# Performance work log

Hardware: AMD Instinct MI355X
Metric: run time of the kernel (lower is better)

## Reference

```python
import jax, jax.numpy as jnp
import numpy as np

TOP_K = 2


def setup_inputs() -> dict:
    key = jax.random.key(0)
    ks = jax.random.split(key, 5)
    T, H, I, E = 4096, 2048, 4096, 8
    scale = 0.02
    return {
        "hidden_states": jax.random.normal(ks[0], (T, H), dtype=jnp.float32),
        "router_logits": jax.random.normal(ks[1], (T, E), dtype=jnp.float32),
        "w1": jax.random.normal(ks[2], (E, I, H), dtype=jnp.float32) * scale,
        "w3": jax.random.normal(ks[3], (E, I, H), dtype=jnp.float32) * scale,
        "w2": jax.random.normal(ks[4], (E, H, I), dtype=jnp.float32) * scale,
    }


def reference(hidden_states, router_logits, w1, w3, w2):
    # hidden_states: [T, H], router_logits: [T, E]
    E = w1.shape[0]
    # Top-k routing with softmax renormalization over the selected logits.
    topk_vals, topk_idx = jax.lax.top_k(router_logits, TOP_K)  # [T, K]
    routing_weights = jax.nn.softmax(topk_vals, axis=-1)       # [T, K]
    # combine[t, e] = sum of routing weights of slots that picked expert e
    combine = jnp.sum(
        jnp.where(topk_idx[:, :, None] == jnp.arange(E)[None, None, :],
                  routing_weights[:, :, None], 0.0),
        axis=1)  # [T, E]
    out = jnp.zeros_like(hidden_states)
    for e in range(E):  # fixed small structural loop over experts
        gate = hidden_states @ w1[e].T        # [T, I]
        up = hidden_states @ w3[e].T          # [T, I]
        y = (jax.nn.silu(gate) * up) @ w2[e].T  # [T, H]
        out = out + combine[:, e, None] * y
    return out
```

## Files before the change

### kernel.cpp

```cpp
#include <hip/hip_runtime.h>
#include <stdint.h>

#define T_TOK 4096
#define H_DIM 2048
#define I_DIM 4096
#define N_EXP 8

typedef __attribute__((ext_vector_type(8))) short bf16x8;
typedef __attribute__((ext_vector_type(4))) float f32x4;
typedef __attribute__((ext_vector_type(8))) unsigned short u16x8;

__device__ __forceinline__ unsigned short f2bf(float x) {
    union { float f; unsigned u; } v; v.f = x;
    unsigned r = v.u + 0x7FFF + ((v.u >> 16) & 1);
    return (unsigned short)(r >> 16);
}

__device__ __forceinline__ u16x8 cvt8(float4 a, float4 b) {
    u16x8 o;
    o[0] = f2bf(a.x); o[1] = f2bf(a.y); o[2] = f2bf(a.z); o[3] = f2bf(a.w);
    o[4] = f2bf(b.x); o[5] = f2bf(b.y); o[6] = f2bf(b.z); o[7] = f2bf(b.w);
    return o;
}

__device__ __forceinline__ void async_cp16(const void* g, const unsigned short* lds_base) {
    __builtin_amdgcn_global_load_lds(
        (const __attribute__((address_space(1))) unsigned*)g,
        (__attribute__((address_space(3))) unsigned*)(unsigned)(uintptr_t)lds_base,
        16, 0, 0);
}

__global__ void routing_kernel(const float* __restrict__ logits,
                               int* __restrict__ counts, int* __restrict__ offsets,
                               int* __restrict__ btok, float* __restrict__ bw,
                               int* __restrict__ tok2slot) {
    __shared__ int s_cnt[N_EXP];
    __shared__ int s_off[N_EXP];
    __shared__ int s_cur[N_EXP];
    const int tid = threadIdx.x;
    if (tid < N_EXP) s_cnt[tid] = 0;
    __syncthreads();

    int e0a[16], e1a[16]; float w0a[16], w1a[16];
    #pragma unroll
    for (int it = 0; it < 16; ++it) {
        int t = tid + it * 256;
        float l[8];
        #pragma unroll
        for (int e = 0; e < 8; ++e) l[e] = logits[t * 8 + e];
        int b0 = 0; float v0 = l[0];
        #pragma unroll
        for (int e = 1; e < 8; ++e) if (l[e] > v0) { v0 = l[e]; b0 = e; }
        int b1 = (b0 == 0) ? 1 : 0; float v1 = l[b1];
        #pragma unroll
        for (int e = 0; e < 8; ++e) if (e != b0 && l[e] > v1) { v1 = l[e]; b1 = e; }
        float w0 = 1.0f / (1.0f + __expf(v1 - v0));
        e0a[it] = b0; e1a[it] = b1; w0a[it] = w0; w1a[it] = 1.0f - w0;
        atomicAdd(&s_cnt[b0], 1);
        atomicAdd(&s_cnt[b1], 1);
    }
    __syncthreads();
    if (tid == 0) {
        int acc = 0;
        for (int e = 0; e < N_EXP; ++e) { s_off[e] = acc; s_cur[e] = acc; acc += s_cnt[e]; }
    }
    __syncthreads();
    if (tid < N_EXP) { counts[tid] = s_cnt[tid]; offsets[tid] = s_off[tid]; }
    #pragma unroll
    for (int it = 0; it < 16; ++it) {
        int t = tid + it * 256;
        int p0 = atomicAdd(&s_cur[e0a[it]], 1);
        btok[p0] = t; bw[p0] = w0a[it];
        int p1 = atomicAdd(&s_cur[e1a[it]], 1);
        btok[p1] = t; bw[p1] = w1a[it];
        tok2slot[2 * t] = p0;
        tok2slot[2 * t + 1] = p1;
    }
}

__global__ void cvt_kernel(const float* __restrict__ x, unsigned short* __restrict__ xb) {
    int i = blockIdx.x * blockDim.x + threadIdx.x;
    float4 a = ((const float4*)x)[2 * i];
    float4 b = ((const float4*)x)[2 * i + 1];
    ((u16x8*)xb)[i] = cvt8(a, b);
}


__global__ __launch_bounds__(512, 2)
void gemm1p_kernel(const unsigned short* __restrict__ Xb,
                   const float* __restrict__ W1,
                   const float* __restrict__ W3,
                   const int* __restrict__ counts,
                   const int* __restrict__ offsets,
                   const int* __restrict__ btok,
                   unsigned short* __restrict__ hbuf) {
    const int e = blockIdx.z;
    const int ne = counts[e];
    const int mt = blockIdx.y;
    if (mt * 256 >= ne) return;
    const int nt = blockIdx.x;
    const int off = offsets[e];

    __shared__ unsigned short sA[4][256 * 32];
    __shared__ unsigned short sB1[4][128 * 32];
    __shared__ unsigned short sB3[4][128 * 32];

    const int tid = threadIdx.x;
    const int lane = tid & 63;
    const int wv = tid >> 6;
    const int wm = (wv >> 1) << 6;
    const int wn = (wv & 1) << 6;
    const int q = lane >> 4;
    const int c = lane & 15;
    const int xq = q ^ ((c >> 1) & 3);

    const int aoff = (wm + c) * 32 + xq * 8;
    const int boff = (wn + c) * 32 + xq * 8;

    const int srow = wv * 16 + (lane >> 2);
    const int sg = (lane & 3) ^ ((lane >> 3) & 3);

    int sl0 = mt * 256 + srow;        if (sl0 >= ne) sl0 = ne - 1;
    int sl1 = mt * 256 + srow + 128;  if (sl1 >= ne) sl1 = ne - 1;
    const int tok0 = btok[off + sl0];
    const int tok1 = btok[off + sl1];

    const unsigned short* gA0 = Xb + (size_t)tok0 * H_DIM + sg * 8;
    const unsigned short* gA1 = Xb + (size_t)tok1 * H_DIM + sg * 8;
    const size_t wrow = (size_t)e * I_DIM + nt * 128 + srow;
    const float* gW1 = W1 + wrow * H_DIM + (lane & 3) * 8;
    const float* gW3 = W3 + wrow * H_DIM + (lane & 3) * 8;
    const int bwro = srow * 32 + sg * 8;

    const int dofsA0 = wv * 512;
    const int dofsA1 = 4096 + wv * 512;

    f32x4 accg[4][4], accu[4][4];
    const f32x4 zero = {0.0f, 0.0f, 0.0f, 0.0f};
    #pragma unroll
    for (int i = 0; i < 4; ++i)
        #pragma unroll
        for (int j = 0; j < 4; ++j) { accg[i][j] = zero; accu[i][j] = zero; }

    {
        float4 a0 = *(const float4*)(gW1);
        float4 a1 = *(const float4*)(gW1 + 4);
        float4 b0 = *(const float4*)(gW3);
        float4 b1 = *(const float4*)(gW3 + 4);
        float4 c0 = *(const float4*)(gW1 + 32);
        float4 c1 = *(const float4*)(gW1 + 36);
        float4 d0 = *(const float4*)(gW3 + 32);
        float4 d1 = *(const float4*)(gW3 + 36);
        *(u16x8*)(&sB1[0][bwro]) = cvt8(a0, a1);
        *(u16x8*)(&sB3[0][bwro]) = cvt8(b0, b1);
        *(u16x8*)(&sB1[1][bwro]) = cvt8(c0, c1);
        *(u16x8*)(&sB3[1][bwro]) = cvt8(d0, d1);
    }
    async_cp16(gA0,      &sA[0][dofsA0]);
    async_cp16(gA1,      &sA[0][dofsA1]);
    async_cp16(gA0 + 32, &sA[1][dofsA0]);
    async_cp16(gA1 + 32, &sA[1][dofsA1]);

    const int NT = H_DIM / 32;
    float4 rc0, rc1, rc2, rc3, rn0, rn1, rn2, rn3;
    rc0 = *(const float4*)(gW1 + 64);
    rc1 = *(const float4*)(gW1 + 68);
    rc2 = *(const float4*)(gW3 + 64);
    rc3 = *(const float4*)(gW3 + 68);

    asm volatile("s_waitcnt lgkmcnt(0)" ::: "memory");
    asm volatile("s_waitcnt vmcnt(6)" ::: "memory");
    __builtin_amdgcn_s_barrier();
    __builtin_amdgcn_sched_barrier(0);

#define G1_PHASE(H, RC0, RC1, RC2, RC3, RN0, RN1, RN2, RN3)                                          \
    {                                                                                                \
        const int cs = (H) & 3;                                                                      \
        if ((H) + 3 < NT) {                                                                          \
            const float* p1 = gW1 + (size_t)((H) + 3) * 32;                                          \
            const float* p3 = gW3 + (size_t)((H) + 3) * 32;                                          \
            RN0 = *(const float4*)(p1);                                                              \
            RN1 = *(const float4*)(p1 + 4);                                                          \
            RN2 = *(const float4*)(p3);                                                              \
            RN3 = *(const float4*)(p3 + 4);                                                          \
        }                                                                                            \
        bf16x8 af[4], b1f[4], b3f[4];                                                                \
        _Pragma("unroll")                                                                            \
        for (int i = 0; i < 4; ++i) af[i]  = *(const bf16x8*)(&sA[cs][aoff + i * 512]);              \
        _Pragma("unroll")                                                                            \
        for (int j = 0; j < 4; ++j) b1f[j] = *(const bf16x8*)(&sB1[cs][boff + j * 512]);             \
        _Pragma("unroll")                                                                            \
        for (int j = 0; j < 4; ++j) b3f[j] = *(const bf16x8*)(&sB3[cs][boff + j * 512]);             \
        if ((H) + 2 < NT) {                                                                          \
            const int ns = ((H) + 2) & 3;                                                            \
            async_cp16(gA0 + ((H) + 2) * 32, &sA[ns][dofsA0]);                                       \
            async_cp16(gA1 + ((H) + 2) * 32, &sA[ns][dofsA1]);                                       \
        }                                                                                            \
        __builtin_amdgcn_sched_barrier(0);                                                           \
        __builtin_amdgcn_s_setprio(1);                                                               \
        _Pragma("unroll")                                                                            \
        for (int i = 0; i < 4; ++i)                                                                  \
            _Pragma("unroll")                                                                        \
            for (int j = 0; j < 4; ++j)                                                              \
                accg[i][j] = __builtin_amdgcn_mfma_f32_16x16x32_bf16(af[i], b1f[j], accg[i][j], 0, 0, 0); \
        _Pragma("unroll")                                                                            \
        for (int i = 0; i < 4; ++i)                                                                  \
            _Pragma("unroll")                                                                        \
            for (int j = 0; j < 4; ++j)                                                              \
                accu[i][j] = __builtin_amdgcn_mfma_f32_16x16x32_bf16(af[i], b3f[j], accu[i][j], 0, 0, 0); \
        __builtin_amdgcn_s_setprio(0);                                                               \
        if ((H) + 2 < NT) {                                                                          \
            const int ns = ((H) + 2) & 3;                                                            \
            *(u16x8*)(&sB1[ns][bwro]) = cvt8(RC0, RC1);                                              \
            *(u16x8*)(&sB3[ns][bwro]) = cvt8(RC2, RC3);                                              \
        }                                                                                            \
        if ((H) + 1 < NT) {                                                                          \
            asm volatile("s_waitcnt lgkmcnt(0)" ::: "memory");                                       \
            if ((H) + 3 < NT)      asm volatile("s_waitcnt vmcnt(6)" ::: "memory");                  \
            else if ((H) + 2 < NT) asm volatile("s_waitcnt vmcnt(2)" ::: "memory");                  \
            else                   asm volatile("s_waitcnt vmcnt(0)" ::: "memory");                  \
            __builtin_amdgcn_s_barrier();                                                            \
            __builtin_amdgcn_sched_barrier(0);                                                       \
        }                                                                                            \
    }

    for (int h = 0; h < NT; h += 2) {
        G1_PHASE(h,     rc0, rc1, rc2, rc3, rn0, rn1, rn2, rn3);
        G1_PHASE(h + 1, rn0, rn1, rn2, rn3, rc0, rc1, rc2, rc3);
    }
#undef G1_PHASE

    #pragma unroll
    for (int i = 0; i < 4; ++i) {
        #pragma unroll
        for (int r = 0; r < 4; ++r) {
            int mloc = wm + i * 16 + q * 4 + r;
            int slot = mt * 256 + mloc;
            if (slot < ne) {
                size_t rowbase = (size_t)(off + slot) * I_DIM + nt * 128 + wn;
                #pragma unroll
                for (int j = 0; j < 4; ++j) {
                    float g = accg[i][j][r];
                    float u = accu[i][j][r];
                    float val = (g / (1.0f + __expf(-g))) * u;
                    hbuf[rowbase + j * 16 + c] = f2bf(val);
                }
            }
        }
    }
}

__global__ __launch_bounds__(512, 2)
void gemm2p_kernel(const unsigned short* __restrict__ hbuf,
                   const float* __restrict__ W2,
                   const int* __restrict__ counts,
                   const int* __restrict__ offsets,
                   float* __restrict__ ybuf) {
    const int e = blockIdx.z;
    const int ne = counts[e];
    const int mt = blockIdx.y;
    if (mt * 256 >= ne) return;
    const int nt = blockIdx.x;
    const int off = offsets[e];

    __shared__ unsigned short sA[4][256 * 32];
    __shared__ unsigned short sB[4][256 * 32];

    const int tid = threadIdx.x;
    const int lane = tid & 63;
    const int wv = tid >> 6;
    const int wm = (wv >> 2) << 7;
    const int wn = (wv & 3) << 6;
    const int q = lane >> 4;
    const int c = lane & 15;
    const int xq = q ^ ((c >> 1) & 3);

    const int aoff = (wm + c) * 32 + xq * 8;
    const int boff = (wn + c) * 32 + xq * 8;

    const int srow = wv * 16 + (lane >> 2);
    const int sg = (lane & 3) ^ ((lane >> 3) & 3);

    int slot0 = mt * 256 + srow;        if (slot0 >= ne) slot0 = ne - 1;
    int slot1 = mt * 256 + srow + 128;  if (slot1 >= ne) slot1 = ne - 1;
    const unsigned short* gA0 = hbuf + (size_t)(off + slot0) * I_DIM + sg * 8;
    const unsigned short* gA1 = hbuf + (size_t)(off + slot1) * I_DIM + sg * 8;
    const size_t wrow = (size_t)e * H_DIM + nt * 256 + srow;
    const float* gB0 = W2 + wrow * I_DIM + (lane & 3) * 8;
    const float* gB1 = gB0 + (size_t)128 * I_DIM;
    const int bwro = srow * 32 + sg * 8;

    const int dofsA0 = wv * 512;
    const int dofsA1 = 4096 + wv * 512;

    f32x4 acc[8][4];
    const f32x4 zero = {0.0f, 0.0f, 0.0f, 0.0f};
    #pragma unroll
    for (int i = 0; i < 8; ++i)
        #pragma unroll
        for (int j = 0; j < 4; ++j) acc[i][j] = zero;

    {
        float4 a0 = *(const float4*)(gB0);
        float4 a1 = *(const float4*)(gB0 + 4);
        float4 b0 = *(const float4*)(gB1);
        float4 b1 = *(const float4*)(gB1 + 4);
        float4 c0 = *(const float4*)(gB0 + 32);
        float4 c1 = *(const float4*)(gB0 + 36);
        float4 d0 = *(const float4*)(gB1 + 32);
        float4 d1 = *(const float4*)(gB1 + 36);
        *(u16x8*)(&sB[0][bwro])        = cvt8(a0, a1);
        *(u16x8*)(&sB[0][bwro + 4096]) = cvt8(b0, b1);
        *(u16x8*)(&sB[1][bwro])        = cvt8(c0, c1);
        *(u16x8*)(&sB[1][bwro + 4096]) = cvt8(d0, d1);
    }
    async_cp16(gA0,      &sA[0][dofsA0]);
    async_cp16(gA1,      &sA[0][dofsA1]);
    async_cp16(gA0 + 32, &sA[1][dofsA0]);
    async_cp16(gA1 + 32, &sA[1][dofsA1]);

    const int NT = I_DIM / 32;
    float4 rc0, rc1, rc2, rc3, rn0, rn1, rn2, rn3;
    rc0 = *(const float4*)(gB0 + 64);
    rc1 = *(const float4*)(gB0 + 68);
    rc2 = *(const float4*)(gB1 + 64);
    rc3 = *(const float4*)(gB1 + 68);

    asm volatile("s_waitcnt lgkmcnt(0)" ::: "memory");
    asm volatile("s_waitcnt vmcnt(6)" ::: "memory");
    __builtin_amdgcn_s_barrier();
    __builtin_amdgcn_sched_barrier(0);

#define G2_PHASE(H, RC0, RC1, RC2, RC3, RN0, RN1, RN2, RN3)                                          \
    {                                                                                                \
        const int cs = (H) & 3;                                                                      \
        if ((H) + 3 < NT) {                                                                          \
            const float* p0 = gB0 + (size_t)((H) + 3) * 32;                                          \
            const float* p1 = gB1 + (size_t)((H) + 3) * 32;                                          \
            RN0 = *(const float4*)(p0);                                                              \
            RN1 = *(const float4*)(p0 + 4);                                                          \
            RN2 = *(const float4*)(p1);                                                              \
            RN3 = *(const float4*)(p1 + 4);                                                          \
        }                                                                                            \
        bf16x8 af[8], bfr[4];                                                                        \
        _Pragma("unroll")                                                                            \
        for (int i = 0; i < 8; ++i) af[i]  = *(const bf16x8*)(&sA[cs][aoff + i * 512]);              \
        _Pragma("unroll")                                                                            \
        for (int j = 0; j < 4; ++j) bfr[j] = *(const bf16x8*)(&sB[cs][boff + j * 512]);              \
        if ((H) + 2 < NT) {                                                                          \
            const int ns = ((H) + 2) & 3;                                                            \
            async_cp16(gA0 + ((H) + 2) * 32, &sA[ns][dofsA0]);                                       \
            async_cp16(gA1 + ((H) + 2) * 32, &sA[ns][dofsA1]);                                       \
        }                                                                                            \
        __builtin_amdgcn_sched_barrier(0);                                                           \
        __builtin_amdgcn_s_setprio(1);                                                               \
        _Pragma("unroll")                                                                            \
        for (int i = 0; i < 8; ++i)                                                                  \
            _Pragma("unroll")                                                                        \
            for (int j = 0; j < 4; ++j)                                                              \
                acc[i][j] = __builtin_amdgcn_mfma_f32_16x16x32_bf16(af[i], bfr[j], acc[i][j], 0, 0, 0); \
        __builtin_amdgcn_s_setprio(0);                                                               \
        if ((H) + 2 < NT) {                                                                          \
            const int ns = ((H) + 2) & 3;                                                            \
            *(u16x8*)(&sB[ns][bwro])        = cvt8(RC0, RC1);                                        \
            *(u16x8*)(&sB[ns][bwro + 4096]) = cvt8(RC2, RC3);                                        \
        }                                                                                            \
        if ((H) + 1 < NT) {                                                                          \
            asm volatile("s_waitcnt lgkmcnt(0)" ::: "memory");                                       \
            if ((H) + 3 < NT)      asm volatile("s_waitcnt vmcnt(6)" ::: "memory");                  \
            else if ((H) + 2 < NT) asm volatile("s_waitcnt vmcnt(2)" ::: "memory");                  \
            else                   asm volatile("s_waitcnt vmcnt(0)" ::: "memory");                  \
            __builtin_amdgcn_s_barrier();                                                            \
            __builtin_amdgcn_sched_barrier(0);                                                       \
        }                                                                                            \
    }

    for (int h = 0; h < NT; h += 2) {
        G2_PHASE(h,     rc0, rc1, rc2, rc3, rn0, rn1, rn2, rn3);
        G2_PHASE(h + 1, rn0, rn1, rn2, rn3, rc0, rc1, rc2, rc3);
    }
#undef G2_PHASE

    #pragma unroll
    for (int i = 0; i < 8; ++i) {
        #pragma unroll
        for (int r = 0; r < 4; ++r) {
            int mloc = wm + i * 16 + q * 4 + r;
            int slot = mt * 256 + mloc;
            if (slot < ne) {
                float* obase = ybuf + (size_t)(off + slot) * H_DIM + nt * 256 + wn;
                #pragma unroll
                for (int j = 0; j < 4; ++j)
                    obase[j * 16 + c] = acc[i][j][r];
            }
        }
    }
}

__global__ void combine_kernel(const float* __restrict__ ybuf,
                               const float* __restrict__ bw,
                               const int* __restrict__ tok2slot,
                               float* __restrict__ out) {
    int i = blockIdx.x * blockDim.x + threadIdx.x;
    int t = i >> 9;
    int h4 = i & 511;
    int p0 = tok2slot[2 * t], p1 = tok2slot[2 * t + 1];
    float w0 = bw[p0], w1 = bw[p1];
    float4 a = ((const float4*)(ybuf + (size_t)p0 * H_DIM))[h4];
    float4 b = ((const float4*)(ybuf + (size_t)p1 * H_DIM))[h4];
    float4 o;
    o.x = w0 * a.x + w1 * b.x;
    o.y = w0 * a.y + w1 * b.y;
    o.z = w0 * a.z + w1 * b.z;
    o.w = w0 * a.w + w1 * b.w;
    ((float4*)(out + (size_t)t * H_DIM))[h4] = o;
}


__global__ __launch_bounds__(256, 2)
void gemm1_kernel(const unsigned short* __restrict__ Xb,
                  const float* __restrict__ W1,
                  const float* __restrict__ W3,
                  const int* __restrict__ counts,
                  const int* __restrict__ offsets,
                  const int* __restrict__ btok,
                  unsigned short* __restrict__ hbuf) {
    const int e = blockIdx.z;
    const int ne = counts[e];
    const int mt = blockIdx.y;
    if (mt * 128 >= ne) return;
    const int nt = blockIdx.x;
    const int off = offsets[e];

    __shared__ unsigned short sA[128][32];
    __shared__ unsigned short sB1[128][32];
    __shared__ unsigned short sB3[128][32];
    __shared__ int s_tok[128];

    const int tid = threadIdx.x;
    if (tid < 128) {
        int slot = mt * 128 + tid;
        s_tok[tid] = (slot < ne) ? btok[off + slot] : -1;
    }

    const float* __restrict__ pB1 = W1 + (size_t)e * I_DIM * H_DIM + (size_t)(nt * 128) * H_DIM;
    const float* __restrict__ pB3 = W3 + (size_t)e * I_DIM * H_DIM + (size_t)(nt * 128) * H_DIM;

    const int lane = tid & 63;
    const int wv = tid >> 6;
    const int wm = (wv >> 1) << 6;
    const int wn = (wv & 1) << 6;
    const int q = lane >> 4;
    const int c = lane & 15;

    f32x4 accg[4][4], accu[4][4];
    const f32x4 zero = {0.0f, 0.0f, 0.0f, 0.0f};
    #pragma unroll
    for (int i = 0; i < 4; ++i)
        #pragma unroll
        for (int j = 0; j < 4; ++j) { accg[i][j] = zero; accu[i][j] = zero; }

    const int srow = tid >> 2;
    const int schunk = (tid & 3) * 8;

    for (int kt = 0; kt < H_DIM; kt += 32) {
        __syncthreads();
        #pragma unroll
        for (int p = 0; p < 2; ++p) {
            int r = srow + p * 64;
            int tok = s_tok[r];
            u16x8 av = {0, 0, 0, 0, 0, 0, 0, 0};
            if (tok >= 0)
                av = *(const u16x8*)(Xb + (size_t)tok * H_DIM + kt + schunk);
            *(u16x8*)(&sA[r][schunk]) = av;

            const float* b1 = pB1 + (size_t)r * H_DIM + kt + schunk;
            *(u16x8*)(&sB1[r][schunk]) = cvt8(*(const float4*)(b1), *(const float4*)(b1 + 4));

            const float* b3 = pB3 + (size_t)r * H_DIM + kt + schunk;
            *(u16x8*)(&sB3[r][schunk]) = cvt8(*(const float4*)(b3), *(const float4*)(b3 + 4));
        }
        __syncthreads();

        bf16x8 af[4], b1f[4], b3f[4];
        #pragma unroll
        for (int i = 0; i < 4; ++i)
            af[i] = *(const bf16x8*)(&sA[wm + i * 16 + c][q * 8]);
        #pragma unroll
        for (int j = 0; j < 4; ++j) {
            b1f[j] = *(const bf16x8*)(&sB1[wn + j * 16 + c][q * 8]);
            b3f[j] = *(const bf16x8*)(&sB3[wn + j * 16 + c][q * 8]);
        }
        #pragma unroll
        for (int i = 0; i < 4; ++i)
            #pragma unroll
            for (int j = 0; j < 4; ++j) {
                accg[i][j] = __builtin_amdgcn_mfma_f32_16x16x32_bf16(af[i], b1f[j], accg[i][j], 0, 0, 0);
                accu[i][j] = __builtin_amdgcn_mfma_f32_16x16x32_bf16(af[i], b3f[j], accu[i][j], 0, 0, 0);
            }
    }

    #pragma unroll
    for (int i = 0; i < 4; ++i) {
        #pragma unroll
        for (int r = 0; r < 4; ++r) {
            int mloc = wm + i * 16 + q * 4 + r;
            int slot = mt * 128 + mloc;
            if (slot < ne) {
                size_t rowbase = (size_t)(off + slot) * I_DIM + nt * 128 + wn;
                #pragma unroll
                for (int j = 0; j < 4; ++j) {
                    float g = accg[i][j][r];
                    float u = accu[i][j][r];
                    float val = (g / (1.0f + __expf(-g))) * u;
                    hbuf[rowbase + j * 16 + c] = f2bf(val);
                }
            }
        }
    }
}

__global__ __launch_bounds__(256, 2)
void gemm2_kernel(const unsigned short* __restrict__ hbuf,
                  const float* __restrict__ W2,
                  const int* __restrict__ counts,
                  const int* __restrict__ offsets,
                  const int* __restrict__ btok,
                  const float* __restrict__ bw,
                  float* __restrict__ out) {
    const int e = blockIdx.z;
    const int ne = counts[e];
    const int mt = blockIdx.y;
    if (mt * 128 >= ne) return;
    const int nt = blockIdx.x;
    const int off = offsets[e];

    __shared__ unsigned short sA[128][32];
    __shared__ unsigned short sB[128][32];

    const int tid = threadIdx.x;
    const int lane = tid & 63;
    const int wv = tid >> 6;
    const int wm = (wv >> 1) << 6;
    const int wn = (wv & 1) << 6;
    const int q = lane >> 4;
    const int c = lane & 15;

    const float* __restrict__ pB = W2 + (size_t)e * H_DIM * I_DIM + (size_t)(nt * 128) * I_DIM;

    f32x4 acc[4][4];
    const f32x4 zero = {0.0f, 0.0f, 0.0f, 0.0f};
    #pragma unroll
    for (int i = 0; i < 4; ++i)
        #pragma unroll
        for (int j = 0; j < 4; ++j) acc[i][j] = zero;

    const int srow = tid >> 2;
    const int schunk = (tid & 3) * 8;

    for (int kt = 0; kt < I_DIM; kt += 32) {
        __syncthreads();
        #pragma unroll
        for (int p = 0; p < 2; ++p) {
            int r = srow + p * 64;
            int slot = mt * 128 + r;
            u16x8 av = {0, 0, 0, 0, 0, 0, 0, 0};
            if (slot < ne)
                av = *(const u16x8*)(hbuf + (size_t)(off + slot) * I_DIM + kt + schunk);
            *(u16x8*)(&sA[r][schunk]) = av;

            const float* b = pB + (size_t)r * I_DIM + kt + schunk;
            *(u16x8*)(&sB[r][schunk]) = cvt8(*(const float4*)(b), *(const float4*)(b + 4));
        }
        __syncthreads();

        bf16x8 af[4], bfr[4];
        #pragma unroll
        for (int i = 0; i < 4; ++i)
            af[i] = *(const bf16x8*)(&sA[wm + i * 16 + c][q * 8]);
        #pragma unroll
        for (int j = 0; j < 4; ++j)
            bfr[j] = *(const bf16x8*)(&sB[wn + j * 16 + c][q * 8]);
        #pragma unroll
        for (int i = 0; i < 4; ++i)
            #pragma unroll
            for (int j = 0; j < 4; ++j)
                acc[i][j] = __builtin_amdgcn_mfma_f32_16x16x32_bf16(af[i], bfr[j], acc[i][j], 0, 0, 0);
    }

    #pragma unroll
    for (int i = 0; i < 4; ++i) {
        #pragma unroll
        for (int r = 0; r < 4; ++r) {
            int mloc = wm + i * 16 + q * 4 + r;
            int slot = mt * 128 + mloc;
            if (slot < ne) {
                int tok = btok[off + slot];
                float wgt = bw[off + slot];
                float* obase = out + (size_t)tok * H_DIM + nt * 128 + wn;
                #pragma unroll
                for (int j = 0; j < 4; ++j)
                    atomicAdd(obase + j * 16 + c, wgt * acc[i][j][r]);
            }
        }
    }
}


extern "C" void kernel_launch(void* const* d_in, const int* in_sizes, int n_in,
                              void* d_out, int out_size, void* d_ws, size_t ws_size,
                              hipStream_t stream) {
    const float* hs = (const float*)d_in[0];
    const float* rl = (const float*)d_in[1];
    const float* w1 = (const float*)d_in[2];
    const float* w3 = (const float*)d_in[3];
    const float* w2 = (const float*)d_in[4];
    float* out = (float*)d_out;

    char* ws = (char*)d_ws;
    int*   counts   = (int*)(ws);
    int*   offsets  = (int*)(ws + 256);
    int*   btok     = (int*)(ws + 4096);
    float* bw       = (float*)(ws + 36864);
    int*   tok2slot = (int*)(ws + 69632);

    const size_t MB = 1ull << 20;
    const size_t NEED_A = 146 * MB;

    if (ws_size >= NEED_A) {
        unsigned short* Xb   = (unsigned short*)(ws + 1 * MB);
        unsigned short* hbuf = (unsigned short*)(ws + 17 * MB);
        float*          ybuf = (float*)(ws + 81 * MB);

        routing_kernel<<<1, 256, 0, stream>>>(rl, counts, offsets, btok, bw, tok2slot);

        cvt_kernel<<<(T_TOK * H_DIM / 8) / 256, 256, 0, stream>>>(hs, Xb);

        gemm1p_kernel<<<dim3(I_DIM / 128, 32, N_EXP), 512, 0, stream>>>(
            Xb, w1, w3, counts, offsets, btok, hbuf);

        gemm2p_kernel<<<dim3(H_DIM / 256, 32, N_EXP), 512, 0, stream>>>(
            hbuf, w2, counts, offsets, ybuf);

        combine_kernel<<<(T_TOK * (H_DIM / 4)) / 256, 256, 0, stream>>>(
            ybuf, bw, tok2slot, out);
    } else {
        unsigned short* Xb   = (unsigned short*)(ws + 1 * MB);
        unsigned short* hbuf = (unsigned short*)(ws + 32 * MB);

        hipMemsetAsync(out, 0, (size_t)T_TOK * H_DIM * sizeof(float), stream);

        routing_kernel<<<1, 256, 0, stream>>>(rl, counts, offsets, btok, bw, tok2slot);

        cvt_kernel<<<(T_TOK * H_DIM / 8) / 256, 256, 0, stream>>>(hs, Xb);

        gemm1_kernel<<<dim3(I_DIM / 128, T_TOK / 128, N_EXP), 256, 0, stream>>>(
            Xb, w1, w3, counts, offsets, btok, hbuf);

        gemm2_kernel<<<dim3(H_DIM / 128, T_TOK / 128, N_EXP), 256, 0, stream>>>(
            hbuf, w2, counts, offsets, btok, bw, out);
    }
}
```

Before: 1.308 ms.

## Shrink MoE GEMM tiles to 128x128 with 256 threads and triple-buffered LDS

Both grouped expert GEMMs move from 512-thread blocks with 256-row token tiles to 256-thread blocks with 128x128 output tiles. The LDS ring drops from four stages to three, and the pipeline is reordered so the fp32-to-bf16 weight conversion is written to LDS at the start of each phase instead of after the MFMAs. The aim is more blocks and better occupancy, plus less wasted work on partially filled expert tiles. In exchange, each fp32 weight tile is fetched and converted twice as often per token, which raises weight traffic from global memory.

```diff
diff --git a/kernel.cpp b/kernel.cpp
--- a/kernel.cpp
+++ b/kernel.cpp
@@ -86,7 +86,7 @@
 }
 
 
-__global__ __launch_bounds__(512, 2)
+__global__ __launch_bounds__(256, 2)
 void gemm1p_kernel(const unsigned short* __restrict__ Xb,
                    const float* __restrict__ W1,
                    const float* __restrict__ W3,
@@ -97,13 +97,13 @@
     const int e = blockIdx.z;
     const int ne = counts[e];
     const int mt = blockIdx.y;
-    if (mt * 256 >= ne) return;
+    if (mt * 128 >= ne) return;
     const int nt = blockIdx.x;
     const int off = offsets[e];
 
-    __shared__ unsigned short sA[4][256 * 32];
-    __shared__ unsigned short sB1[4][128 * 32];
-    __shared__ unsigned short sB3[4][128 * 32];
+    __shared__ unsigned short sA[3][128 * 32];
+    __shared__ unsigned short sB1[3][128 * 32];
+    __shared__ unsigned short sB3[3][128 * 32];
 
     const int tid = threadIdx.x;
     const int lane = tid & 63;
@@ -117,23 +117,25 @@
     const int aoff = (wm + c) * 32 + xq * 8;
     const int boff = (wn + c) * 32 + xq * 8;
 
-    const int srow = wv * 16 + (lane >> 2);
-    const int sg = (lane & 3) ^ ((lane >> 3) & 3);
-
-    int sl0 = mt * 256 + srow;        if (sl0 >= ne) sl0 = ne - 1;
-    int sl1 = mt * 256 + srow + 128;  if (sl1 >= ne) sl1 = ne - 1;
-    const int tok0 = btok[off + sl0];
-    const int tok1 = btok[off + sl1];
-
-    const unsigned short* gA0 = Xb + (size_t)tok0 * H_DIM + sg * 8;
-    const unsigned short* gA1 = Xb + (size_t)tok1 * H_DIM + sg * 8;
-    const size_t wrow = (size_t)e * I_DIM + nt * 128 + srow;
-    const float* gW1 = W1 + wrow * H_DIM + (lane & 3) * 8;
-    const float* gW3 = W3 + wrow * H_DIM + (lane & 3) * 8;
-    const int bwro = srow * 32 + sg * 8;
-
+    const int arow = wv * 16 + (lane >> 2);
+    const int sgA = (lane & 3) ^ ((lane >> 3) & 3);
+
+    int sl0 = mt * 128 + arow;       if (sl0 >= ne) sl0 = ne - 1;
+    int sl1 = mt * 128 + arow + 64;  if (sl1 >= ne) sl1 = ne - 1;
+    const unsigned short* gA0 = Xb + (size_t)btok[off + sl0] * H_DIM + sgA * 8;
+    const unsigned short* gA1 = Xb + (size_t)btok[off + sl1] * H_DIM + sgA * 8;
     const int dofsA0 = wv * 512;
-    const int dofsA1 = 4096 + wv * 512;
+    const int dofsA1 = 2048 + wv * 512;
+
+    const int brow = tid >> 2;
+    const int sgB = (tid & 3) ^ ((tid >> 3) & 3);
+    const size_t wrow = (size_t)e * I_DIM + nt * 128 + brow;
+    const float* gW1  = W1 + wrow * H_DIM + (tid & 3) * 8;
+    const float* gW1b = gW1 + (size_t)64 * H_DIM;
+    const float* gW3  = W3 + wrow * H_DIM + (tid & 3) * 8;
+    const float* gW3b = gW3 + (size_t)64 * H_DIM;
+    const int bwro  = brow * 32 + sgB * 8;
+    const int bwro2 = bwro + 2048;
 
     f32x4 accg[4][4], accu[4][4];
     const f32x4 zero = {0.0f, 0.0f, 0.0f, 0.0f};
@@ -142,59 +144,63 @@
         #pragma unroll
         for (int j = 0; j < 4; ++j) { accg[i][j] = zero; accu[i][j] = zero; }
 
-    {
-        float4 a0 = *(const float4*)(gW1);
-        float4 a1 = *(const float4*)(gW1 + 4);
-        float4 b0 = *(const float4*)(gW3);
-        float4 b1 = *(const float4*)(gW3 + 4);
-        float4 c0 = *(const float4*)(gW1 + 32);
-        float4 c1 = *(const float4*)(gW1 + 36);
-        float4 d0 = *(const float4*)(gW3 + 32);
-        float4 d1 = *(const float4*)(gW3 + 36);
-        *(u16x8*)(&sB1[0][bwro]) = cvt8(a0, a1);
-        *(u16x8*)(&sB3[0][bwro]) = cvt8(b0, b1);
-        *(u16x8*)(&sB1[1][bwro]) = cvt8(c0, c1);
-        *(u16x8*)(&sB3[1][bwro]) = cvt8(d0, d1);
+    float4 w0, w1, w2, w3, w4, w5, w6, w7;
+
+    #pragma unroll
+    for (int h = 0; h < 2; ++h) {
+        const float* p1  = gW1  + h * 32;
+        const float* p1b = gW1b + h * 32;
+        const float* p3  = gW3  + h * 32;
+        const float* p3b = gW3b + h * 32;
+        *(u16x8*)(&sB1[h][bwro])  = cvt8(((const float4*)p1)[0],  ((const float4*)p1)[1]);
+        *(u16x8*)(&sB1[h][bwro2]) = cvt8(((const float4*)p1b)[0], ((const float4*)p1b)[1]);
+        *(u16x8*)(&sB3[h][bwro])  = cvt8(((const float4*)p3)[0],  ((const float4*)p3)[1]);
+        *(u16x8*)(&sB3[h][bwro2]) = cvt8(((const float4*)p3b)[0], ((const float4*)p3b)[1]);
     }
     async_cp16(gA0,      &sA[0][dofsA0]);
     async_cp16(gA1,      &sA[0][dofsA1]);
     async_cp16(gA0 + 32, &sA[1][dofsA0]);
     async_cp16(gA1 + 32, &sA[1][dofsA1]);
-
-    const int NT = H_DIM / 32;
-    float4 rc0, rc1, rc2, rc3, rn0, rn1, rn2, rn3;
-    rc0 = *(const float4*)(gW1 + 64);
-    rc1 = *(const float4*)(gW1 + 68);
-    rc2 = *(const float4*)(gW3 + 64);
-    rc3 = *(const float4*)(gW3 + 68);
+    w0 = ((const float4*)(gW1  + 64))[0]; w1 = ((const float4*)(gW1  + 64))[1];
+    w2 = ((const float4*)(gW1b + 64))[0]; w3 = ((const float4*)(gW1b + 64))[1];
+    w4 = ((const float4*)(gW3  + 64))[0]; w5 = ((const float4*)(gW3  + 64))[1];
+    w6 = ((const float4*)(gW3b + 64))[0]; w7 = ((const float4*)(gW3b + 64))[1];
 
     asm volatile("s_waitcnt lgkmcnt(0)" ::: "memory");
-    asm volatile("s_waitcnt vmcnt(6)" ::: "memory");
+    asm volatile("s_waitcnt vmcnt(10)" ::: "memory");
     __builtin_amdgcn_s_barrier();
     __builtin_amdgcn_sched_barrier(0);
 
-#define G1_PHASE(H, RC0, RC1, RC2, RC3, RN0, RN1, RN2, RN3)                                          \
+    const int NT = H_DIM / 32;
+
+#define G1_PH(H, S, S2)                                                                              \
     {                                                                                                \
-        const int cs = (H) & 3;                                                                      \
+        if ((H) + 2 < NT) {                                                                          \
+            *(u16x8*)(&sB1[S2][bwro])  = cvt8(w0, w1);                                               \
+            *(u16x8*)(&sB1[S2][bwro2]) = cvt8(w2, w3);                                               \
+            *(u16x8*)(&sB3[S2][bwro])  = cvt8(w4, w5);                                               \
+            *(u16x8*)(&sB3[S2][bwro2]) = cvt8(w6, w7);                                               \
+        }                                                                                            \
         if ((H) + 3 < NT) {                                                                          \
-            const float* p1 = gW1 + (size_t)((H) + 3) * 32;                                          \
-            const float* p3 = gW3 + (size_t)((H) + 3) * 32;                                          \
-            RN0 = *(const float4*)(p1);                                                              \
-            RN1 = *(const float4*)(p1 + 4);                                                          \
-            RN2 = *(const float4*)(p3);                                                              \
-            RN3 = *(const float4*)(p3 + 4);                                                          \
+            const float* p1  = gW1  + (size_t)((H) + 3) * 32;                                        \
+            const float* p1b = gW1b + (size_t)((H) + 3) * 32;                                        \
+            const float* p3  = gW3  + (size_t)((H) + 3) * 32;                                        \
+            const float* p3b = gW3b + (size_t)((H) + 3) * 32;                                        \
+            w0 = ((const float4*)p1)[0];  w1 = ((const float4*)p1)[1];                               \
+            w2 = ((const float4*)p1b)[0]; w3 = ((const float4*)p1b)[1];                              \
+            w4 = ((const float4*)p3)[0];  w5 = ((const float4*)p3)[1];                               \
+            w6 = ((const float4*)p3b)[0]; w7 = ((const float4*)p3b)[1];                              \
         }                                                                                            \
         bf16x8 af[4], b1f[4], b3f[4];                                                                \
         _Pragma("unroll")                                                                            \
-        for (int i = 0; i < 4; ++i) af[i]  = *(const bf16x8*)(&sA[cs][aoff + i * 512]);              \
-        _Pragma("unroll")                                                                            \
-        for (int j = 0; j < 4; ++j) b1f[j] = *(const bf16x8*)(&sB1[cs][boff + j * 512]);             \
-        _Pragma("unroll")                                                                            \
-        for (int j = 0; j < 4; ++j) b3f[j] = *(const bf16x8*)(&sB3[cs][boff + j * 512]);             \
+        for (int i = 0; i < 4; ++i) af[i]  = *(const bf16x8*)(&sA[S][aoff + i * 512]);               \
+        _Pragma("unroll")                                                                            \
+        for (int j = 0; j < 4; ++j) b1f[j] = *(const bf16x8*)(&sB1[S][boff + j * 512]);              \
+        _Pragma("unroll")                                                                            \
+        for (int j = 0; j < 4; ++j) b3f[j] = *(const bf16x8*)(&sB3[S][boff + j * 512]);              \
         if ((H) + 2 < NT) {                                                                          \
-            const int ns = ((H) + 2) & 3;                                                            \
-            async_cp16(gA0 + ((H) + 2) * 32, &sA[ns][dofsA0]);                                       \
-            async_cp16(gA1 + ((H) + 2) * 32, &sA[ns][dofsA1]);                                       \
+            async_cp16(gA0 + ((H) + 2) * 32, &sA[S2][dofsA0]);                                       \
+            async_cp16(gA1 + ((H) + 2) * 32, &sA[S2][dofsA1]);                                       \
         }                                                                                            \
         __builtin_amdgcn_sched_barrier(0);                                                           \
         __builtin_amdgcn_s_setprio(1);                                                               \
@@ -209,14 +215,9 @@
             for (int j = 0; j < 4; ++j)                                                              \
                 accu[i][j] = __builtin_amdgcn_mfma_f32_16x16x32_bf16(af[i], b3f[j], accu[i][j], 0, 0, 0); \
         __builtin_amdgcn_s_setprio(0);                                                               \
-        if ((H) + 2 < NT) {                                                                          \
-            const int ns = ((H) + 2) & 3;                                                            \
-            *(u16x8*)(&sB1[ns][bwro]) = cvt8(RC0, RC1);                                              \
-            *(u16x8*)(&sB3[ns][bwro]) = cvt8(RC2, RC3);                                              \
-        }                                                                                            \
         if ((H) + 1 < NT) {                                                                          \
             asm volatile("s_waitcnt lgkmcnt(0)" ::: "memory");                                       \
-            if ((H) + 3 < NT)      asm volatile("s_waitcnt vmcnt(6)" ::: "memory");                  \
+            if ((H) + 3 < NT)      asm volatile("s_waitcnt vmcnt(10)" ::: "memory");                 \
             else if ((H) + 2 < NT) asm volatile("s_waitcnt vmcnt(2)" ::: "memory");                  \
             else                   asm volatile("s_waitcnt vmcnt(0)" ::: "memory");                  \
             __builtin_amdgcn_s_barrier();                                                            \
@@ -224,18 +225,22 @@
         }                                                                                            \
     }
 
-    for (int h = 0; h < NT; h += 2) {
-        G1_PHASE(h,     rc0, rc1, rc2, rc3, rn0, rn1, rn2, rn3);
-        G1_PHASE(h + 1, rn0, rn1, rn2, rn3, rc0, rc1, rc2, rc3);
-    }
-#undef G1_PHASE
+    int h = 0;
+    for (int t = 0; t < 21; ++t) {
+        G1_PH(h,     0, 2);
+        G1_PH(h + 1, 1, 0);
+        G1_PH(h + 2, 2, 1);
+        h += 3;
+    }
+    G1_PH(63, 0, 2);
+#undef G1_PH
 
     #pragma unroll
     for (int i = 0; i < 4; ++i) {
         #pragma unroll
         for (int r = 0; r < 4; ++r) {
             int mloc = wm + i * 16 + q * 4 + r;
-            int slot = mt * 256 + mloc;
+            int slot = mt * 128 + mloc;
             if (slot < ne) {
                 size_t rowbase = (size_t)(off + slot) * I_DIM + nt * 128 + wn;
                 #pragma unroll
@@ -250,7 +255,7 @@
     }
 }
 
-__global__ __launch_bounds__(512, 2)
+__global__ __launch_bounds__(256, 3)
 void gemm2p_kernel(const unsigned short* __restrict__ hbuf,
                    const float* __restrict__ W2,
                    const int* __restrict__ counts,
@@ -259,18 +264,18 @@
     const int e = blockIdx.z;
     const int ne = counts[e];
     const int mt = blockIdx.y;
-    if (mt * 256 >= ne) return;
+    if (mt * 128 >= ne) return;
     const int nt = blockIdx.x;
     const int off = offsets[e];
 
-    __shared__ unsigned short sA[4][256 * 32];
-    __shared__ unsigned short sB[4][256 * 32];
+    __shared__ unsigned short sA[3][128 * 32];
+    __shared__ unsigned short sB[3][128 * 32];
 
     const int tid = threadIdx.x;
     const int lane = tid & 63;
     const int wv = tid >> 6;
-    const int wm = (wv >> 2) << 7;
-    const int wn = (wv & 3) << 6;
+    const int wm = (wv >> 1) << 6;
+    const int wn = (wv & 1) << 6;
     const int q = lane >> 4;
     const int c = lane & 15;
     const int xq = q ^ ((c >> 1) & 3);
@@ -278,93 +283,82 @@
     const int aoff = (wm + c) * 32 + xq * 8;
     const int boff = (wn + c) * 32 + xq * 8;
 
-    const int srow = wv * 16 + (lane >> 2);
-    const int sg = (lane & 3) ^ ((lane >> 3) & 3);
-
-    int slot0 = mt * 256 + srow;        if (slot0 >= ne) slot0 = ne - 1;
-    int slot1 = mt * 256 + srow + 128;  if (slot1 >= ne) slot1 = ne - 1;
-    const unsigned short* gA0 = hbuf + (size_t)(off + slot0) * I_DIM + sg * 8;
-    const unsigned short* gA1 = hbuf + (size_t)(off + slot1) * I_DIM + sg * 8;
-    const size_t wrow = (size_t)e * H_DIM + nt * 256 + srow;
-    const float* gB0 = W2 + wrow * I_DIM + (lane & 3) * 8;
-    const float* gB1 = gB0 + (size_t)128 * I_DIM;
-    const int bwro = srow * 32 + sg * 8;
-
+    const int arow = wv * 16 + (lane >> 2);
+    const int sgA = (lane & 3) ^ ((lane >> 3) & 3);
+    int sl0 = mt * 128 + arow;       if (sl0 >= ne) sl0 = ne - 1;
+    int sl1 = mt * 128 + arow + 64;  if (sl1 >= ne) sl1 = ne - 1;
+    const unsigned short* gA0 = hbuf + (size_t)(off + sl0) * I_DIM + sgA * 8;
+    const unsigned short* gA1 = hbuf + (size_t)(off + sl1) * I_DIM + sgA * 8;
     const int dofsA0 = wv * 512;
-    const int dofsA1 = 4096 + wv * 512;
-
-    f32x4 acc[8][4];
+    const int dofsA1 = 2048 + wv * 512;
+
+    const int brow = tid >> 2;
+    const int sgB = (tid & 3) ^ ((tid >> 3) & 3);
+    const size_t wrow = (size_t)e * H_DIM + nt * 128 + brow;
+    const float* gB  = W2 + wrow * I_DIM + (tid & 3) * 8;
+    const float* gBb = gB + (size_t)64 * I_DIM;
+    const int bwro  = brow * 32 + sgB * 8;
+    const int bwro2 = bwro + 2048;
+
+    f32x4 acc[4][4];
     const f32x4 zero = {0.0f, 0.0f, 0.0f, 0.0f};
     #pragma unroll
-    for (int i = 0; i < 8; ++i)
+    for (int i = 0; i < 4; ++i)
         #pragma unroll
         for (int j = 0; j < 4; ++j) acc[i][j] = zero;
 
-    {
-        float4 a0 = *(const float4*)(gB0);
-        float4 a1 = *(const float4*)(gB0 + 4);
-        float4 b0 = *(const float4*)(gB1);
-        float4 b1 = *(const float4*)(gB1 + 4);
-        float4 c0 = *(const float4*)(gB0 + 32);
-        float4 c1 = *(const float4*)(gB0 + 36);
-        float4 d0 = *(const float4*)(gB1 + 32);
-        float4 d1 = *(const float4*)(gB1 + 36);
-        *(u16x8*)(&sB[0][bwro])        = cvt8(a0, a1);
-        *(u16x8*)(&sB[0][bwro + 4096]) = cvt8(b0, b1);
-        *(u16x8*)(&sB[1][bwro])        = cvt8(c0, c1);
-        *(u16x8*)(&sB[1][bwro + 4096]) = cvt8(d0, d1);
+    float4 w0, w1, w2, w3;
+
+    #pragma unroll
+    for (int h = 0; h < 2; ++h) {
+        const float* p  = gB  + h * 32;
+        const float* pb = gBb + h * 32;
+        *(u16x8*)(&sB[h][bwro])  = cvt8(((const float4*)p)[0],  ((const float4*)p)[1]);
+        *(u16x8*)(&sB[h][bwro2]) = cvt8(((const float4*)pb)[0], ((const float4*)pb)[1]);
     }
     async_cp16(gA0,      &sA[0][dofsA0]);
     async_cp16(gA1,      &sA[0][dofsA1]);
     async_cp16(gA0 + 32, &sA[1][dofsA0]);
     async_cp16(gA1 + 32, &sA[1][dofsA1]);
-
-    const int NT = I_DIM / 32;
-    float4 rc0, rc1, rc2, rc3, rn0, rn1, rn2, rn3;
-    rc0 = *(const float4*)(gB0 + 64);
-    rc1 = *(const float4*)(gB0 + 68);
-    rc2 = *(const float4*)(gB1 + 64);
-    rc3 = *(const float4*)(gB1 + 68);
+    w0 = ((const float4*)(gB  + 64))[0]; w1 = ((const float4*)(gB  + 64))[1];
+    w2 = ((const float4*)(gBb + 64))[0]; w3 = ((const float4*)(gBb + 64))[1];
 
     asm volatile("s_waitcnt lgkmcnt(0)" ::: "memory");
     asm volatile("s_waitcnt vmcnt(6)" ::: "memory");
     __builtin_amdgcn_s_barrier();
     __builtin_amdgcn_sched_barrier(0);
 
-#define G2_PHASE(H, RC0, RC1, RC2, RC3, RN0, RN1, RN2, RN3)                                          \
+    const int NT = I_DIM / 32;
+
+#define G2_PH(H, S, S2)                                                                              \
     {                                                                                                \
-        const int cs = (H) & 3;                                                                      \
+        if ((H) + 2 < NT) {                                                                          \
+            *(u16x8*)(&sB[S2][bwro])  = cvt8(w0, w1);                                                \
+            *(u16x8*)(&sB[S2][bwro2]) = cvt8(w2, w3);                                                \
+        }                                                                                            \
         if ((H) + 3 < NT) {                                                                          \
-            const float* p0 = gB0 + (size_t)((H) + 3) * 32;                                          \
-            const float* p1 = gB1 + (size_t)((H) + 3) * 32;                                          \
-            RN0 = *(const float4*)(p0);                                                              \
-            RN1 = *(const float4*)(p0 + 4);                                                          \
-            RN2 = *(const float4*)(p1);                                                              \
-            RN3 = *(const float4*)(p1 + 4);                                                          \
-        }                                                                                            \
-        bf16x8 af[8], bfr[4];                                                                        \
-        _Pragma("unroll")                                                                            \
-        for (int i = 0; i < 8; ++i) af[i]  = *(const bf16x8*)(&sA[cs][aoff + i * 512]);              \
-        _Pragma("unroll")                                                                            \
-        for (int j = 0; j < 4; ++j) bfr[j] = *(const bf16x8*)(&sB[cs][boff + j * 512]);              \
+            const float* p  = gB  + (size_t)((H) + 3) * 32;                                          \
+            const float* pb = gBb + (size_t)((H) + 3) * 32;                                          \
+            w0 = ((const float4*)p)[0];  w1 = ((const float4*)p)[1];                                 \
+            w2 = ((const float4*)pb)[0]; w3 = ((const float4*)pb)[1];                                \
+        }                                                                                            \
+        bf16x8 af[4], bfr[4];                                                                        \
+        _Pragma("unroll")                                                                            \
+        for (int i = 0; i < 4; ++i) af[i]  = *(const bf16x8*)(&sA[S][aoff + i * 512]);               \
+        _Pragma("unroll")                                                                            \
+        for (int j = 0; j < 4; ++j) bfr[j] = *(const bf16x8*)(&sB[S][boff + j * 512]);               \
         if ((H) + 2 < NT) {                                                                          \
-            const int ns = ((H) + 2) & 3;                                                            \
-            async_cp16(gA0 + ((H) + 2) * 32, &sA[ns][dofsA0]);                                       \
-            async_cp16(gA1 + ((H) + 2) * 32, &sA[ns][dofsA1]);                                       \
+            async_cp16(gA0 + ((H) + 2) * 32, &sA[S2][dofsA0]);                                       \
+            async_cp16(gA1 + ((H) + 2) * 32, &sA[S2][dofsA1]);                                       \
         }                                                                                            \
         __builtin_amdgcn_sched_barrier(0);                                                           \
         __builtin_amdgcn_s_setprio(1);                                                               \
         _Pragma("unroll")                                                                            \
-        for (int i = 0; i < 8; ++i)                                                                  \
+        for (int i = 0; i < 4; ++i)                                                                  \
             _Pragma("unroll")                                                                        \
             for (int j = 0; j < 4; ++j)                                                              \
                 acc[i][j] = __builtin_amdgcn_mfma_f32_16x16x32_bf16(af[i], bfr[j], acc[i][j], 0, 0, 0); \
         __builtin_amdgcn_s_setprio(0);                                                               \
-        if ((H) + 2 < NT) {                                                                          \
-            const int ns = ((H) + 2) & 3;                                                            \
-            *(u16x8*)(&sB[ns][bwro])        = cvt8(RC0, RC1);                                        \
-            *(u16x8*)(&sB[ns][bwro + 4096]) = cvt8(RC2, RC3);                                        \
-        }                                                                                            \
         if ((H) + 1 < NT) {                                                                          \
             asm volatile("s_waitcnt lgkmcnt(0)" ::: "memory");                                       \
             if ((H) + 3 < NT)      asm volatile("s_waitcnt vmcnt(6)" ::: "memory");                  \
@@ -375,20 +369,25 @@
         }                                                                                            \
     }
 
-    for (int h = 0; h < NT; h += 2) {
-        G2_PHASE(h,     rc0, rc1, rc2, rc3, rn0, rn1, rn2, rn3);
-        G2_PHASE(h + 1, rn0, rn1, rn2, rn3, rc0, rc1, rc2, rc3);
-    }
-#undef G2_PHASE
-
-    #pragma unroll
-    for (int i = 0; i < 8; ++i) {
+    int h = 0;
+    for (int t = 0; t < 42; ++t) {
+        G2_PH(h,     0, 2);
+        G2_PH(h + 1, 1, 0);
+        G2_PH(h + 2, 2, 1);
+        h += 3;
+    }
+    G2_PH(126, 0, 2);
+    G2_PH(127, 1, 0);
+#undef G2_PH
+
+    #pragma unroll
+    for (int i = 0; i < 4; ++i) {
         #pragma unroll
         for (int r = 0; r < 4; ++r) {
             int mloc = wm + i * 16 + q * 4 + r;
-            int slot = mt * 256 + mloc;
+            int slot = mt * 128 + mloc;
             if (slot < ne) {
-                float* obase = ybuf + (size_t)(off + slot) * H_DIM + nt * 256 + wn;
+                float* obase = ybuf + (size_t)(off + slot) * H_DIM + nt * 128 + wn;
                 #pragma unroll
                 for (int j = 0; j < 4; ++j)
                     obase[j * 16 + c] = acc[i][j][r];
@@ -636,10 +635,10 @@
 
         cvt_kernel<<<(T_TOK * H_DIM / 8) / 256, 256, 0, stream>>>(hs, Xb);
 
-        gemm1p_kernel<<<dim3(I_DIM / 128, 32, N_EXP), 512, 0, stream>>>(
+        gemm1p_kernel<<<dim3(I_DIM / 128, 64, N_EXP), 256, 0, stream>>>(
             Xb, w1, w3, counts, offsets, btok, hbuf);
 
-        gemm2p_kernel<<<dim3(H_DIM / 256, 32, N_EXP), 512, 0, stream>>>(
+        gemm2p_kernel<<<dim3(H_DIM / 128, 64, N_EXP), 256, 0, stream>>>(
             hbuf, w2, counts, offsets, ybuf);
 
         combine_kernel<<<(T_TOK * (H_DIM / 4)) / 256, 256, 0, stream>>>(
```

Result: faster. 1.235 ms (-5.6%).
